# Optimization experiments

Measured on AMD Instinct MI355X. Metric: run time of the kernel, lower is better.

## Reference

```python
import jax, jax.numpy as jnp
import numpy as np

FD, NH, SP, GS = 256, 4, 2, 80.0
E = FD // NH
SP3 = SP ** 3


def _bilinear(plane, uv):
    # plane: [B,C,H,W], uv: [B,N,2] in [0,1] -> [B,C,N] (align_corners=True style)
    B, C, H, W = plane.shape
    x = jnp.clip(uv[..., 0], 0.0, 1.0) * (W - 1)
    y = jnp.clip(uv[..., 1], 0.0, 1.0) * (H - 1)
    x0 = jnp.floor(x); y0 = jnp.floor(y)
    wx = (x - x0)[:, None, :]; wy = (y - y0)[:, None, :]
    x0i = x0.astype(jnp.int32); y0i = y0.astype(jnp.int32)
    x1i = jnp.minimum(x0i + 1, W - 1); y1i = jnp.minimum(y0i + 1, H - 1)
    g = jax.vmap(lambda pl, yy, xx: pl[:, yy, xx])  # per-batch gather -> [C,N]
    f00 = g(plane, y0i, x0i); f01 = g(plane, y0i, x1i)
    f10 = g(plane, y1i, x0i); f11 = g(plane, y1i, x1i)
    return (f00 * (1 - wy) * (1 - wx) + f01 * (1 - wy) * wx
            + f10 * wy * (1 - wx) + f11 * wy * wx)


def _triplane(p, c_xz, c_xy, c_yz):
    # p: [B,N,3] in [0,1] -> [B,N,FD]; sum of three plane samples (ConvONet style)
    px, py, pz = p[..., 0], p[..., 1], p[..., 2]
    f = (_bilinear(c_xz, jnp.stack([px, pz], -1))
         + _bilinear(c_xy, jnp.stack([px, py], -1))
         + _bilinear(c_yz, jnp.stack([py, pz], -1)))
    return jnp.swapaxes(f, 1, 2)


def setup_inputs() -> dict:
    key = jax.random.key(0)
    ks = jax.random.split(key, 10)
    bs, ns, H = 4, 1024, 128
    inp = {}
    inp['query_pos'] = jax.random.uniform(ks[0], (bs, ns, 3), dtype=jnp.float32)
    for i, nm in enumerate(['c_xz', 'c_xy', 'c_yz']):
        inp[nm] = jax.random.normal(ks[1 + i], (bs, FD, H, H), dtype=jnp.float32)

    def lin(k, fi, fo):  # xavier-uniform like torch init
        lim = (6.0 / (fi + fo)) ** 0.5
        return jax.random.uniform(k, (fi, fo), minval=-lim, maxval=lim, dtype=jnp.float32)

    # to_offset: small random weight (torch inits to 0; small noise exercises the path),
    # bias = normalized sp^3 anchor grid / grid_scale, tiled over heads (as in __init__)
    inp['w_off'] = 0.01 * jax.random.normal(ks[4], (FD, SP3 * NH * 3), dtype=jnp.float32)
    g = np.stack(np.meshgrid(np.arange(SP), np.arange(SP), np.arange(SP), indexing='ij'), axis=-1).astype(np.float32)
    gsc = (2.0 * g / max(SP - 1, 1) - 1.0) / GS  # [sp,sp,sp,3]
    inp['b_off'] = jnp.asarray(np.tile(gsc[:, :, :, None, :], (1, 1, 1, NH, 1)).reshape(-1))
    inp['w_q'] = lin(ks[5], FD, E); inp['b_q'] = jnp.zeros((E,), jnp.float32)
    inp['w_k'] = lin(ks[6], FD, E); inp['b_k'] = jnp.zeros((E,), jnp.float32)
    inp['w_v'] = lin(ks[7], FD, E); inp['b_v'] = jnp.zeros((E,), jnp.float32)
    inp['w_out'] = lin(ks[8], FD, FD); inp['b_out'] = jnp.zeros((FD,), jnp.float32)
    return inp


def reference(query_pos, c_xz, c_xy, c_yz, w_off, b_off, w_q, b_q, w_k, b_k, w_v, b_v, w_out, b_out):
    bs, ns, _ = query_pos.shape
    feature = _triplane(query_pos, c_xz, c_xy, c_yz)                 # [bs,ns,FD]
    off = (feature @ w_off + b_off).reshape(bs, ns, SP3, NH, 3)
    aux = off + query_pos[:, :, None, None, :]                        # [bs,ns,SP3,NH,3]
    aux_feat = _triplane(aux.reshape(bs, -1, 3), c_xz, c_xy, c_yz)
    aux_feat = aux_feat.reshape(bs * ns, SP3, NH, FD)
    k = jnp.swapaxes(aux_feat @ w_k + b_k, 1, 2)                      # [bn,NH,SP3,E]
    v = jnp.swapaxes(aux_feat @ w_v + b_v, 1, 2)
    # note: original does q / scale with scale = E**-0.5, i.e. q * sqrt(E)
    q = (feature @ w_q + b_q).reshape(bs * ns, 1, 1, E) * (E ** 0.5)
    q = jnp.broadcast_to(q, (bs * ns, NH, 1, E))
    sim = jnp.einsum('bnid,bnjd->bnij', q, k)                         # [bn,NH,1,SP3]
    attn = jax.nn.softmax(sim, axis=-1)                               # dropout = identity (eval)
    out = jnp.einsum('bnij,bnjd->bnid', attn, v)                      # [bn,NH,1,E]
    out = jnp.swapaxes(out, 1, 2).reshape(bs, ns, NH * E)
    return out @ w_out + b_out + feature
```

## Files before the change

### kernel.cpp

```cpp
#include <hip/hip_runtime.h>
#include <math.h>

#define FD   256
#define NH   4
#define SP3  8
#define NP   32
#define EDIM 64
#define H    128
#define NS   1024
#define BS   4
#define QT   8

#define TEX         (H*H)
#define BATCH_ELEMS (TEX*FD)
#define PAIR_B      2
#define PAIR_Q      (PAIR_B*NS)
#define PPLANE      (PAIR_B*BATCH_ELEMS)

#define WS_PLANES 0
#define WS_FEAT   (3*PPLANE)
#define WS_QK     (WS_FEAT + PAIR_Q*FD)
#define WS_AUX    (WS_QK   + PAIR_Q*FD)
#define WS_WF     (WS_AUX  + PAIR_Q*NP*3)
#define WS_PERM   (WS_WF   + PAIR_Q*NH*FD)

__device__ __forceinline__ unsigned short f2bf(float f) {
  unsigned b = __float_as_uint(f);
  return (unsigned short)((b + 0x7FFFu + ((b >> 16) & 1u)) >> 16);
}
__device__ __forceinline__ float bf2f(unsigned short u) {
  return __uint_as_float(((unsigned)u) << 16);
}

__global__ __launch_bounds__(256) void tpk2(
    const float* __restrict__ xz, const float* __restrict__ xy,
    const float* __restrict__ yz, float* __restrict__ dstAll, int b0)
{
  int bid = blockIdx.x;
  int tT = bid & 511; bid >>= 9;
  int bl = bid & 1;   bid >>= 1;
  int pl = bid;
  const float* src = pl == 0 ? xz : (pl == 1 ? xy : yz);
  float* dst = dstAll + (size_t)pl * PPLANE + (size_t)bl * BATCH_ELEMS;
  int b = b0 + bl;

  __shared__ float T[32 * 260];
  int lane = threadIdx.x & 63, w = threadIdx.x >> 6;
  int tex4 = (lane & 7) * 4;
  int csub = lane >> 3;

  const float* sbase = src + (size_t)b * FD * TEX + tT * 32;
  #pragma unroll
  for (int i = 0; i < 8; i++) {
    int c = i * 32 + w * 8 + csub;
    float4 v = *(const float4*)(sbase + (size_t)c * TEX + tex4);
    T[(tex4 + 0) * 260 + c] = v.x;
    T[(tex4 + 1) * 260 + c] = v.y;
    T[(tex4 + 2) * 260 + c] = v.z;
    T[(tex4 + 3) * 260 + c] = v.w;
  }
  __syncthreads();
  #pragma unroll
  for (int i = 0; i < 8; i++) {
    int t = w * 8 + i;
    float4 v = *(const float4*)(&T[t * 260 + lane * 4]);
    *(float4*)(dst + (size_t)(tT * 32 + t) * FD + lane * 4) = v;
  }
}

__device__ __forceinline__ unsigned mort7(unsigned v) {
  unsigned r = 0;
  #pragma unroll
  for (int i = 0; i < 7; i++) r |= ((v >> i) & 1u) << (3 * i);
  return r;
}

__global__ __launch_bounds__(1024) void sortk(
    const float* __restrict__ qpos, unsigned* __restrict__ perm)
{
  const int pair = blockIdx.x;
  const int b0 = pair * PAIR_B;
  const int t = threadIdx.x;
  __shared__ unsigned cnt[256];
  __shared__ unsigned base[256];
  if (t < 256) cnt[t] = 0;
  __syncthreads();
  unsigned myb[2];
  #pragma unroll
  for (int r = 0; r < 2; r++) {
    int i = t + r * 1024;
    size_t qg = (size_t)b0 * NS + i;
    float x = fminf(fmaxf(qpos[qg * 3 + 0], 0.f), 1.f);
    float y = fminf(fmaxf(qpos[qg * 3 + 1], 0.f), 1.f);
    float z = fminf(fmaxf(qpos[qg * 3 + 2], 0.f), 1.f);
    unsigned m = (mort7((unsigned)(x * 127.f)) << 2)
               | (mort7((unsigned)(y * 127.f)) << 1)
               |  mort7((unsigned)(z * 127.f));
    unsigned bkt = ((unsigned)(i >> 10) << 7) | (m >> 14);
    myb[r] = bkt;
    atomicAdd(&cnt[bkt], 1u);
  }
  __syncthreads();
  if (t == 0) {
    unsigned s = 0;
    for (int k = 0; k < 256; k++) { base[k] = s; s += cnt[k]; }
  }
  __syncthreads();
  #pragma unroll
  for (int r = 0; r < 2; r++) {
    int i = t + r * 1024;
    unsigned pos = atomicAdd(&base[myb[r]], 1u);
    perm[(size_t)pair * PAIR_Q + pos] = (unsigned)i;
  }
}

__device__ __forceinline__ float sample_plane(const float* __restrict__ p,
                                              float u, float v) {
  float x = fminf(fmaxf(u, 0.f), 1.f) * (float)(H - 1);
  float y = fminf(fmaxf(v, 0.f), 1.f) * (float)(H - 1);
  float xf = floorf(x), yf = floorf(y);
  int x0 = (int)xf, y0 = (int)yf;
  float wx = x - xf, wy = y - yf;
  int dx = (x0 < H - 1) ? FD : 0;
  int dy = (y0 < H - 1) ? H * FD : 0;
  int i00 = (y0 * H + x0) * FD;
  float f00 = p[i00], f01 = p[i00 + dx], f10 = p[i00 + dy], f11 = p[i00 + dy + dx];
  float a = f00 + wx * (f01 - f00);
  float b = f10 + wx * (f11 - f10);
  return a + wy * (b - a);
}

__device__ __forceinline__ void setup_samp(int* si, float* sw, float u, float v) {
  float x = fminf(fmaxf(u, 0.f), 1.f) * (float)(H - 1);
  float y = fminf(fmaxf(v, 0.f), 1.f) * (float)(H - 1);
  float xf = floorf(x), yf = floorf(y);
  int x0 = (int)xf, y0 = (int)yf;
  float wx = x - xf, wy = y - yf;
  si[0] = (y0 * H + x0) * FD;
  si[1] = (x0 < H - 1) ? FD : 0;
  si[2] = (y0 < H - 1) ? H * FD : 0;
  sw[0] = (1.f - wy) * (1.f - wx);
  sw[1] = (1.f - wy) * wx;
  sw[2] = wy * (1.f - wx);
  sw[3] = wy * wx;
}

__global__ __launch_bounds__(256) void featk(
    const float* __restrict__ qpos, const float* __restrict__ planesT,
    const float* __restrict__ w_off, const float* __restrict__ b_off,
    const float* __restrict__ w_q, const float* __restrict__ b_q,
    const float* __restrict__ w_k,
    float* __restrict__ feat, float* __restrict__ aux, float* __restrict__ qk,
    int b0)
{
  const int tid = threadIdx.x;
  const int q0l = blockIdx.x * QT;
  const int bl = q0l >> 10;
  __shared__ float s_feat[QT * 260];
  __shared__ float s_q[QT * 68];

  const float* Pxz = planesT + 0 * (size_t)PPLANE + (size_t)bl * BATCH_ELEMS + tid;
  const float* Pxy = planesT + 1 * (size_t)PPLANE + (size_t)bl * BATCH_ELEMS + tid;
  const float* Pyz = planesT + 2 * (size_t)PPLANE + (size_t)bl * BATCH_ELEMS + tid;

  for (int qs = 0; qs < QT; qs++) {
    size_t qg = (size_t)b0 * NS + q0l + qs;
    float px = qpos[qg * 3 + 0], py = qpos[qg * 3 + 1], pz = qpos[qg * 3 + 2];
    float f = sample_plane(Pxz, px, pz) + sample_plane(Pxy, px, py)
            + sample_plane(Pyz, py, pz);
    s_feat[qs * 260 + tid] = f;
    feat[(size_t)(q0l + qs) * FD + tid] = f;
  }
  __syncthreads();

  if (tid < 192) {
    int half = tid / 96, j = tid - half * 96;
    float acc[4];
    float bj = b_off[j];
    #pragma unroll
    for (int k = 0; k < 4; k++) acc[k] = bj;
    for (int c = 0; c < FD; c++) {
      float wv = w_off[c * 96 + j];
      #pragma unroll
      for (int k = 0; k < 4; k++)
        acc[k] = fmaf(s_feat[(half * 4 + k) * 260 + c], wv, acc[k]);
    }
    int d = j % 3;
    #pragma unroll
    for (int k = 0; k < 4; k++) {
      int qs = half * 4 + k;
      size_t qg = (size_t)b0 * NS + q0l + qs;
      aux[(size_t)(q0l + qs) * 96 + j] = acc[k] + qpos[qg * 3 + d];
    }
  }
  {
    int e = tid & 63, g = tid >> 6;
    #pragma unroll
    for (int k = 0; k < 2; k++) {
      int qs = g * 2 + k;
      float a = b_q[e];
      for (int c = 0; c < FD; c++)
        a = fmaf(s_feat[qs * 260 + c], w_q[c * EDIM + e], a);
      s_q[qs * 68 + e] = a * 8.0f;
    }
  }
  __syncthreads();
  {
    float acc[QT];
    #pragma unroll
    for (int qs = 0; qs < QT; qs++) acc[qs] = 0.f;
    const float4* wk4 = reinterpret_cast<const float4*>(w_k + (size_t)tid * EDIM);
    for (int e4 = 0; e4 < EDIM / 4; e4++) {
      float4 wv = wk4[e4];
      int e = e4 * 4;
      #pragma unroll
      for (int qs = 0; qs < QT; qs++) {
        acc[qs] = fmaf(s_q[qs * 68 + e + 0], wv.x, acc[qs]);
        acc[qs] = fmaf(s_q[qs * 68 + e + 1], wv.y, acc[qs]);
        acc[qs] = fmaf(s_q[qs * 68 + e + 2], wv.z, acc[qs]);
        acc[qs] = fmaf(s_q[qs * 68 + e + 3], wv.w, acc[qs]);
      }
    }
    #pragma unroll
    for (int qs = 0; qs < QT; qs++)
      qk[(size_t)(q0l + qs) * FD + tid] = acc[qs];
  }
}

__global__ __launch_bounds__(256) void attnk(
    const float* __restrict__ planesT, const float* __restrict__ aux,
    const float* __restrict__ qk, const unsigned* __restrict__ perm,
    float* __restrict__ wf)
{
  const int tid = threadIdx.x, lane = tid & 63, w = tid >> 6;
  const int bid = blockIdx.x;
  const int j = ((bid & 7) << 7) | (bid >> 3);
  const int c4 = lane * 4;

  __shared__ int     s_si[2][96][3];
  __shared__ float   s_sw[2][96][4];
  __shared__ float   s_sim[2][NP];
  __shared__ float   s_attn[2][NP];
  __shared__ ushort4 s_af[2 * NP * 64];
  __shared__ int     s_q[2];

  if (tid < 2) s_q[tid] = (int)perm[2 * j + tid];
  __syncthreads();
  const int qw = s_q[w >> 1];
  const int blw = qw >> 10;

  if (tid < 192) {
    int qi = tid / 96, r = tid - qi * 96;
    int p = r / 3, pl = r - p * 3;
    int qq = s_q[qi];
    float ax = aux[(size_t)qq * 96 + p * 3 + 0];
    float ay = aux[(size_t)qq * 96 + p * 3 + 1];
    float az = aux[(size_t)qq * 96 + p * 3 + 2];
    float u = (pl == 2) ? ay : ax;
    float v = (pl == 1) ? ay : az;
    setup_samp(s_si[qi][r], s_sw[qi][r], u, v);
  }
  float4 qk4 = *(const float4*)(qk + (size_t)qw * FD + c4);
  const float* P0 = planesT + 0 * (size_t)PPLANE + (size_t)blw * BATCH_ELEMS + c4;
  const float* P1 = planesT + 1 * (size_t)PPLANE + (size_t)blw * BATCH_ELEMS + c4;
  const float* P2 = planesT + 2 * (size_t)PPLANE + (size_t)blw * BATCH_ELEMS + c4;
  __syncthreads();

  const int qi = w >> 1;
  #pragma unroll 2
  for (int k = 0; k < 16; k++) {
    int p = (w & 1) * 16 + k;
    float4 a; a.x = 0.f; a.y = 0.f; a.z = 0.f; a.w = 0.f;
    #pragma unroll
    for (int pl = 0; pl < 3; pl++) {
      const float* P = pl == 0 ? P0 : (pl == 1 ? P1 : P2);
      int i00 = s_si[qi][p * 3 + pl][0];
      int dxo = s_si[qi][p * 3 + pl][1];
      int dyo = s_si[qi][p * 3 + pl][2];
      float w0 = s_sw[qi][p * 3 + pl][0], w1 = s_sw[qi][p * 3 + pl][1];
      float w2 = s_sw[qi][p * 3 + pl][2], w3 = s_sw[qi][p * 3 + pl][3];
      float4 f00 = *(const float4*)(P + i00);
      float4 f01 = *(const float4*)(P + i00 + dxo);
      float4 f10 = *(const float4*)(P + i00 + dyo);
      float4 f11 = *(const float4*)(P + i00 + dyo + dxo);
      a.x = fmaf(w0, f00.x, fmaf(w1, f01.x, fmaf(w2, f10.x, fmaf(w3, f11.x, a.x))));
      a.y = fmaf(w0, f00.y, fmaf(w1, f01.y, fmaf(w2, f10.y, fmaf(w3, f11.y, a.y))));
      a.z = fmaf(w0, f00.z, fmaf(w1, f01.z, fmaf(w2, f10.z, fmaf(w3, f11.z, a.z))));
      a.w = fmaf(w0, f00.w, fmaf(w1, f01.w, fmaf(w2, f10.w, fmaf(w3, f11.w, a.w))));
    }
    ushort4 h;
    h.x = f2bf(a.x); h.y = f2bf(a.y); h.z = f2bf(a.z); h.w = f2bf(a.w);
    s_af[(qi * NP + p) * 64 + lane] = h;
    float t = fmaf(qk4.x, a.x, fmaf(qk4.y, a.y, fmaf(qk4.z, a.z, qk4.w * a.w)));
    #pragma unroll
    for (int o = 32; o >= 1; o >>= 1) t += __shfl_xor(t, o, 64);
    if (lane == 0) s_sim[qi][p] = t;
  }
  __syncthreads();

  if (tid < 2 * NH) {
    int si = tid >> 2, h = tid & 3;
    float sim[SP3], m = -1e30f;
    #pragma unroll
    for (int jj = 0; jj < SP3; jj++) { sim[jj] = s_sim[si][jj * NH + h]; m = fmaxf(m, sim[jj]); }
    float sum = 0.f, e_[SP3];
    #pragma unroll
    for (int jj = 0; jj < SP3; jj++) { e_[jj] = __expf(sim[jj] - m); sum += e_[jj]; }
    float inv = 1.0f / sum;
    #pragma unroll
    for (int jj = 0; jj < SP3; jj++) s_attn[si][jj * NH + h] = e_[jj] * inv;
  }
  __syncthreads();

  {
    #pragma unroll
    for (int hi = 0; hi < 2; hi++) {
      int h = (w & 1) + hi * 2;
      float4 r; r.x = 0.f; r.y = 0.f; r.z = 0.f; r.w = 0.f;
      #pragma unroll
      for (int jj = 0; jj < SP3; jj++) {
        int p = jj * NH + h;
        float a = s_attn[qi][p];
        ushort4 hv = s_af[(qi * NP + p) * 64 + lane];
        r.x = fmaf(a, bf2f(hv.x), r.x);
        r.y = fmaf(a, bf2f(hv.y), r.y);
        r.z = fmaf(a, bf2f(hv.z), r.z);
        r.w = fmaf(a, bf2f(hv.w), r.w);
      }
      *(float4*)(wf + ((size_t)qw * NH + h) * FD + c4) = r;
    }
  }
}

__global__ __launch_bounds__(256) void epik(
    const float* __restrict__ wf, const float* __restrict__ feat,
    const float* __restrict__ w_v, const float* __restrict__ b_v,
    const float* __restrict__ w_out, const float* __restrict__ b_out,
    float* __restrict__ out, int b0)
{
  const int tid = threadIdx.x;
  const int q0l = blockIdx.x * QT;
  __shared__ float s_wv[FD * EDIM];
  __shared__ float s_o[QT * 257];

  {
    const float4* src4 = (const float4*)w_v;
    float4* dst4 = (float4*)s_wv;
    #pragma unroll
    for (int i = 0; i < (FD * EDIM / 4) / 256; i++)
      dst4[tid + 256 * i] = src4[tid + 256 * i];
  }
  __syncthreads();

  {
    int h = tid >> 6, e = tid & 63;
    float acc[QT];
    float bv = b_v[e];
    #pragma unroll
    for (int qs = 0; qs < QT; qs++) acc[qs] = bv;
    const float* wrow = wf + ((size_t)q0l * NH + h) * FD;
    for (int c = 0; c < FD; c++) {
      float wv = s_wv[c * EDIM + e];
      #pragma unroll
      for (int qs = 0; qs < QT; qs++)
        acc[qs] = fmaf(wrow[(size_t)qs * NH * FD + c], wv, acc[qs]);
    }
    #pragma unroll
    for (int qs = 0; qs < QT; qs++) s_o[qs * 257 + h * EDIM + e] = acc[qs];
  }
  __syncthreads();

  {
    float r[QT];
    float bo = b_out[tid];
    #pragma unroll
    for (int qs = 0; qs < QT; qs++) r[qs] = bo;
    for (int c = 0; c < FD; c++) {
      float wv = w_out[(size_t)c * FD + tid];
      #pragma unroll
      for (int qs = 0; qs < QT; qs++)
        r[qs] = fmaf(s_o[qs * 257 + c], wv, r[qs]);
    }
    #pragma unroll
    for (int qs = 0; qs < QT; qs++)
      out[((size_t)b0 * NS + q0l + qs) * FD + tid]
          = r[qs] + feat[(size_t)(q0l + qs) * FD + tid];
  }
}

extern "C" void kernel_launch(void* const* d_in, const int* in_sizes, int n_in,
                              void* d_out, int out_size, void* d_ws, size_t ws_size,
                              hipStream_t stream) {
  const float* qp    = (const float*)d_in[0];
  const float* cxz   = (const float*)d_in[1];
  const float* cxy   = (const float*)d_in[2];
  const float* cyz   = (const float*)d_in[3];
  const float* w_off = (const float*)d_in[4];
  const float* b_off = (const float*)d_in[5];
  const float* w_q   = (const float*)d_in[6];
  const float* b_q   = (const float*)d_in[7];
  const float* w_k   = (const float*)d_in[8];
  const float* b_k   = (const float*)d_in[9];   (void)b_k;
  const float* w_v   = (const float*)d_in[10];
  const float* b_v   = (const float*)d_in[11];
  const float* w_out = (const float*)d_in[12];
  const float* b_out = (const float*)d_in[13];
  float* out = (float*)d_out;
  (void)in_sizes; (void)n_in; (void)out_size; (void)ws_size;

  float* ws      = (float*)d_ws;
  float* planesT = ws + WS_PLANES;
  float* feat    = ws + WS_FEAT;
  float* qk      = ws + WS_QK;
  float* aux     = ws + WS_AUX;
  float* wf      = ws + WS_WF;
  unsigned* perm = (unsigned*)(ws + WS_PERM);

  hipLaunchKernelGGL(sortk, dim3(BS / PAIR_B), dim3(1024), 0, stream, qp, perm);

  for (int pair = 0; pair < BS / PAIR_B; ++pair) {
    int b0 = pair * PAIR_B;
    hipLaunchKernelGGL(tpk2, dim3(3 * PAIR_B * 512), dim3(256), 0, stream,
                       cxz, cxy, cyz, planesT, b0);
    hipLaunchKernelGGL(featk, dim3(PAIR_Q / QT), dim3(256), 0, stream,
                       qp, planesT, w_off, b_off, w_q, b_q, w_k,
                       feat, aux, qk, b0);
    hipLaunchKernelGGL(attnk, dim3(PAIR_Q / 2), dim3(256), 0, stream,
                       planesT, aux, qk, perm + (size_t)pair * PAIR_Q, wf);
    hipLaunchKernelGGL(epik, dim3(PAIR_Q / QT), dim3(256), 0, stream,
                       wf, feat, w_v, b_v, w_out, b_out, out, b0);
  }
}
```

Baseline: 538.9 us.

## Restructure attention kernel to per-wave softmax in registers, shrink query tiles

The attention kernel now has each wave handle one query's head pair end to end. It keeps the bf16 samples and similarity scores in registers and computes the softmax locally, which removes the shared-memory staging buffers and two block-wide barriers. It also adds a min-blocks-per-CU launch bound to raise occupancy. The feature and epilogue kernels halve their per-block query tile from 8 to 4, doubling the grid size at the cost of less weight reuse per block. The register-resident arrays could raise register pressure or cause spills under the occupancy bound.

```diff
diff --git a/kernel.cpp b/kernel.cpp
--- a/kernel.cpp
+++ b/kernel.cpp
@@ -9,7 +9,8 @@
 #define H    128
 #define NS   1024
 #define BS   4
-#define QT   8
+#define QTF  4
+#define QTE  4
 
 #define TEX         (H*H)
 #define BATCH_ELEMS (TEX*FD)
@@ -154,16 +155,16 @@
     int b0)
 {
   const int tid = threadIdx.x;
-  const int q0l = blockIdx.x * QT;
+  const int q0l = blockIdx.x * QTF;
   const int bl = q0l >> 10;
-  __shared__ float s_feat[QT * 260];
-  __shared__ float s_q[QT * 68];
+  __shared__ float s_feat[QTF * 260];
+  __shared__ float s_q[QTF * 68];
 
   const float* Pxz = planesT + 0 * (size_t)PPLANE + (size_t)bl * BATCH_ELEMS + tid;
   const float* Pxy = planesT + 1 * (size_t)PPLANE + (size_t)bl * BATCH_ELEMS + tid;
   const float* Pyz = planesT + 2 * (size_t)PPLANE + (size_t)bl * BATCH_ELEMS + tid;
 
-  for (int qs = 0; qs < QT; qs++) {
+  for (int qs = 0; qs < QTF; qs++) {
     size_t qg = (size_t)b0 * NS + q0l + qs;
     float px = qpos[qg * 3 + 0], py = qpos[qg * 3 + 1], pz = qpos[qg * 3 + 2];
     float f = sample_plane(Pxz, px, pz) + sample_plane(Pxy, px, py)
@@ -175,46 +176,41 @@
 
   if (tid < 192) {
     int half = tid / 96, j = tid - half * 96;
-    float acc[4];
+    float acc[2];
     float bj = b_off[j];
-    #pragma unroll
-    for (int k = 0; k < 4; k++) acc[k] = bj;
+    acc[0] = bj; acc[1] = bj;
     for (int c = 0; c < FD; c++) {
       float wv = w_off[c * 96 + j];
       #pragma unroll
-      for (int k = 0; k < 4; k++)
-        acc[k] = fmaf(s_feat[(half * 4 + k) * 260 + c], wv, acc[k]);
+      for (int k = 0; k < 2; k++)
+        acc[k] = fmaf(s_feat[(half * 2 + k) * 260 + c], wv, acc[k]);
     }
     int d = j % 3;
     #pragma unroll
-    for (int k = 0; k < 4; k++) {
-      int qs = half * 4 + k;
+    for (int k = 0; k < 2; k++) {
+      int qs = half * 2 + k;
       size_t qg = (size_t)b0 * NS + q0l + qs;
       aux[(size_t)(q0l + qs) * 96 + j] = acc[k] + qpos[qg * 3 + d];
     }
   }
   {
     int e = tid & 63, g = tid >> 6;
-    #pragma unroll
-    for (int k = 0; k < 2; k++) {
-      int qs = g * 2 + k;
-      float a = b_q[e];
-      for (int c = 0; c < FD; c++)
-        a = fmaf(s_feat[qs * 260 + c], w_q[c * EDIM + e], a);
-      s_q[qs * 68 + e] = a * 8.0f;
-    }
+    float a = b_q[e];
+    for (int c = 0; c < FD; c++)
+      a = fmaf(s_feat[g * 260 + c], w_q[c * EDIM + e], a);
+    s_q[g * 68 + e] = a * 8.0f;
   }
   __syncthreads();
   {
-    float acc[QT];
-    #pragma unroll
-    for (int qs = 0; qs < QT; qs++) acc[qs] = 0.f;
+    float acc[QTF];
+    #pragma unroll
+    for (int qs = 0; qs < QTF; qs++) acc[qs] = 0.f;
     const float4* wk4 = reinterpret_cast<const float4*>(w_k + (size_t)tid * EDIM);
     for (int e4 = 0; e4 < EDIM / 4; e4++) {
       float4 wv = wk4[e4];
       int e = e4 * 4;
       #pragma unroll
-      for (int qs = 0; qs < QT; qs++) {
+      for (int qs = 0; qs < QTF; qs++) {
         acc[qs] = fmaf(s_q[qs * 68 + e + 0], wv.x, acc[qs]);
         acc[qs] = fmaf(s_q[qs * 68 + e + 1], wv.y, acc[qs]);
         acc[qs] = fmaf(s_q[qs * 68 + e + 2], wv.z, acc[qs]);
@@ -222,12 +218,12 @@
       }
     }
     #pragma unroll
-    for (int qs = 0; qs < QT; qs++)
+    for (int qs = 0; qs < QTF; qs++)
       qk[(size_t)(q0l + qs) * FD + tid] = acc[qs];
   }
 }
 
-__global__ __launch_bounds__(256) void attnk(
+__global__ __launch_bounds__(256, 6) void attnk(
     const float* __restrict__ planesT, const float* __restrict__ aux,
     const float* __restrict__ qk, const unsigned* __restrict__ perm,
     float* __restrict__ wf)
@@ -237,98 +233,83 @@
   const int j = ((bid & 7) << 7) | (bid >> 3);
   const int c4 = lane * 4;
 
-  __shared__ int     s_si[2][96][3];
-  __shared__ float   s_sw[2][96][4];
-  __shared__ float   s_sim[2][NP];
-  __shared__ float   s_attn[2][NP];
-  __shared__ ushort4 s_af[2 * NP * 64];
-  __shared__ int     s_q[2];
-
-  if (tid < 2) s_q[tid] = (int)perm[2 * j + tid];
-  __syncthreads();
-  const int qw = s_q[w >> 1];
-  const int blw = qw >> 10;
+  __shared__ int   s_si[2][96][3];
+  __shared__ float s_sw[2][96][4];
 
   if (tid < 192) {
-    int qi = tid / 96, r = tid - qi * 96;
+    int qi_s = tid / 96, r = tid - qi_s * 96;
     int p = r / 3, pl = r - p * 3;
-    int qq = s_q[qi];
+    int qq = (int)perm[2 * j + qi_s];
     float ax = aux[(size_t)qq * 96 + p * 3 + 0];
     float ay = aux[(size_t)qq * 96 + p * 3 + 1];
     float az = aux[(size_t)qq * 96 + p * 3 + 2];
     float u = (pl == 2) ? ay : ax;
     float v = (pl == 1) ? ay : az;
-    setup_samp(s_si[qi][r], s_sw[qi][r], u, v);
-  }
+    setup_samp(s_si[qi_s][r], s_sw[qi_s][r], u, v);
+  }
+
+  const int qi = w >> 1;
+  const int h0 = w & 1;
+  const int qw = (int)perm[2 * j + qi];
+  const int blw = qw >> 10;
   float4 qk4 = *(const float4*)(qk + (size_t)qw * FD + c4);
   const float* P0 = planesT + 0 * (size_t)PPLANE + (size_t)blw * BATCH_ELEMS + c4;
   const float* P1 = planesT + 1 * (size_t)PPLANE + (size_t)blw * BATCH_ELEMS + c4;
   const float* P2 = planesT + 2 * (size_t)PPLANE + (size_t)blw * BATCH_ELEMS + c4;
   __syncthreads();
 
-  const int qi = w >> 1;
-  #pragma unroll 2
-  for (int k = 0; k < 16; k++) {
-    int p = (w & 1) * 16 + k;
-    float4 a; a.x = 0.f; a.y = 0.f; a.z = 0.f; a.w = 0.f;
-    #pragma unroll
-    for (int pl = 0; pl < 3; pl++) {
-      const float* P = pl == 0 ? P0 : (pl == 1 ? P1 : P2);
-      int i00 = s_si[qi][p * 3 + pl][0];
-      int dxo = s_si[qi][p * 3 + pl][1];
-      int dyo = s_si[qi][p * 3 + pl][2];
-      float w0 = s_sw[qi][p * 3 + pl][0], w1 = s_sw[qi][p * 3 + pl][1];
-      float w2 = s_sw[qi][p * 3 + pl][2], w3 = s_sw[qi][p * 3 + pl][3];
-      float4 f00 = *(const float4*)(P + i00);
-      float4 f01 = *(const float4*)(P + i00 + dxo);
-      float4 f10 = *(const float4*)(P + i00 + dyo);
-      float4 f11 = *(const float4*)(P + i00 + dyo + dxo);
-      a.x = fmaf(w0, f00.x, fmaf(w1, f01.x, fmaf(w2, f10.x, fmaf(w3, f11.x, a.x))));
-      a.y = fmaf(w0, f00.y, fmaf(w1, f01.y, fmaf(w2, f10.y, fmaf(w3, f11.y, a.y))));
-      a.z = fmaf(w0, f00.z, fmaf(w1, f01.z, fmaf(w2, f10.z, fmaf(w3, f11.z, a.z))));
-      a.w = fmaf(w0, f00.w, fmaf(w1, f01.w, fmaf(w2, f10.w, fmaf(w3, f11.w, a.w))));
-    }
-    ushort4 h;
-    h.x = f2bf(a.x); h.y = f2bf(a.y); h.z = f2bf(a.z); h.w = f2bf(a.w);
-    s_af[(qi * NP + p) * 64 + lane] = h;
-    float t = fmaf(qk4.x, a.x, fmaf(qk4.y, a.y, fmaf(qk4.z, a.z, qk4.w * a.w)));
-    #pragma unroll
-    for (int o = 32; o >= 1; o >>= 1) t += __shfl_xor(t, o, 64);
-    if (lane == 0) s_sim[qi][p] = t;
-  }
-  __syncthreads();
-
-  if (tid < 2 * NH) {
-    int si = tid >> 2, h = tid & 3;
-    float sim[SP3], m = -1e30f;
-    #pragma unroll
-    for (int jj = 0; jj < SP3; jj++) { sim[jj] = s_sim[si][jj * NH + h]; m = fmaxf(m, sim[jj]); }
-    float sum = 0.f, e_[SP3];
-    #pragma unroll
-    for (int jj = 0; jj < SP3; jj++) { e_[jj] = __expf(sim[jj] - m); sum += e_[jj]; }
+  #pragma unroll
+  for (int hi = 0; hi < 2; hi++) {
+    const int h = h0 + 2 * hi;
+    ushort4 af16[SP3];
+    float sim[SP3];
+    #pragma unroll 2
+    for (int jj = 0; jj < SP3; jj++) {
+      const int p = jj * NH + h;
+      float4 a; a.x = 0.f; a.y = 0.f; a.z = 0.f; a.w = 0.f;
+      #pragma unroll
+      for (int pl = 0; pl < 3; pl++) {
+        const float* P = pl == 0 ? P0 : (pl == 1 ? P1 : P2);
+        int i00 = s_si[qi][p * 3 + pl][0];
+        int dxo = s_si[qi][p * 3 + pl][1];
+        int dyo = s_si[qi][p * 3 + pl][2];
+        float w0 = s_sw[qi][p * 3 + pl][0], w1 = s_sw[qi][p * 3 + pl][1];
+        float w2 = s_sw[qi][p * 3 + pl][2], w3 = s_sw[qi][p * 3 + pl][3];
+        float4 f00 = *(const float4*)(P + i00);
+        float4 f01 = *(const float4*)(P + i00 + dxo);
+        float4 f10 = *(const float4*)(P + i00 + dyo);
+        float4 f11 = *(const float4*)(P + i00 + dyo + dxo);
+        a.x = fmaf(w0, f00.x, fmaf(w1, f01.x, fmaf(w2, f10.x, fmaf(w3, f11.x, a.x))));
+        a.y = fmaf(w0, f00.y, fmaf(w1, f01.y, fmaf(w2, f10.y, fmaf(w3, f11.y, a.y))));
+        a.z = fmaf(w0, f00.z, fmaf(w1, f01.z, fmaf(w2, f10.z, fmaf(w3, f11.z, a.z))));
+        a.w = fmaf(w0, f00.w, fmaf(w1, f01.w, fmaf(w2, f10.w, fmaf(w3, f11.w, a.w))));
+      }
+      ushort4 hh;
+      hh.x = f2bf(a.x); hh.y = f2bf(a.y); hh.z = f2bf(a.z); hh.w = f2bf(a.w);
+      af16[jj] = hh;
+      float t = fmaf(qk4.x, a.x, fmaf(qk4.y, a.y, fmaf(qk4.z, a.z, qk4.w * a.w)));
+      #pragma unroll
+      for (int o = 32; o >= 1; o >>= 1) t += __shfl_xor(t, o, 64);
+      sim[jj] = t;
+    }
+    float m = -1e30f;
+    #pragma unroll
+    for (int jj = 0; jj < SP3; jj++) m = fmaxf(m, sim[jj]);
+    float sum = 0.f;
+    #pragma unroll
+    for (int jj = 0; jj < SP3; jj++) { sim[jj] = __expf(sim[jj] - m); sum += sim[jj]; }
     float inv = 1.0f / sum;
-    #pragma unroll
-    for (int jj = 0; jj < SP3; jj++) s_attn[si][jj * NH + h] = e_[jj] * inv;
-  }
-  __syncthreads();
-
-  {
-    #pragma unroll
-    for (int hi = 0; hi < 2; hi++) {
-      int h = (w & 1) + hi * 2;
-      float4 r; r.x = 0.f; r.y = 0.f; r.z = 0.f; r.w = 0.f;
-      #pragma unroll
-      for (int jj = 0; jj < SP3; jj++) {
-        int p = jj * NH + h;
-        float a = s_attn[qi][p];
-        ushort4 hv = s_af[(qi * NP + p) * 64 + lane];
-        r.x = fmaf(a, bf2f(hv.x), r.x);
-        r.y = fmaf(a, bf2f(hv.y), r.y);
-        r.z = fmaf(a, bf2f(hv.z), r.z);
-        r.w = fmaf(a, bf2f(hv.w), r.w);
-      }
-      *(float4*)(wf + ((size_t)qw * NH + h) * FD + c4) = r;
-    }
+    float4 r; r.x = 0.f; r.y = 0.f; r.z = 0.f; r.w = 0.f;
+    #pragma unroll
+    for (int jj = 0; jj < SP3; jj++) {
+      float av = sim[jj] * inv;
+      ushort4 hv = af16[jj];
+      r.x = fmaf(av, bf2f(hv.x), r.x);
+      r.y = fmaf(av, bf2f(hv.y), r.y);
+      r.z = fmaf(av, bf2f(hv.z), r.z);
+      r.w = fmaf(av, bf2f(hv.w), r.w);
+    }
+    *(float4*)(wf + ((size_t)qw * NH + h) * FD + c4) = r;
   }
 }
 
@@ -339,9 +320,9 @@
     float* __restrict__ out, int b0)
 {
   const int tid = threadIdx.x;
-  const int q0l = blockIdx.x * QT;
+  const int q0l = blockIdx.x * QTE;
   __shared__ float s_wv[FD * EDIM];
-  __shared__ float s_o[QT * 257];
+  __shared__ float s_o[QTE * 257];
 
   {
     const float4* src4 = (const float4*)w_v;
@@ -354,35 +335,35 @@
 
   {
     int h = tid >> 6, e = tid & 63;
-    float acc[QT];
+    float acc[QTE];
     float bv = b_v[e];
     #pragma unroll
-    for (int qs = 0; qs < QT; qs++) acc[qs] = bv;
+    for (int qs = 0; qs < QTE; qs++) acc[qs] = bv;
     const float* wrow = wf + ((size_t)q0l * NH + h) * FD;
     for (int c = 0; c < FD; c++) {
       float wv = s_wv[c * EDIM + e];
       #pragma unroll
-      for (int qs = 0; qs < QT; qs++)
+      for (int qs = 0; qs < QTE; qs++)
         acc[qs] = fmaf(wrow[(size_t)qs * NH * FD + c], wv, acc[qs]);
     }
     #pragma unroll
-    for (int qs = 0; qs < QT; qs++) s_o[qs * 257 + h * EDIM + e] = acc[qs];
+    for (int qs = 0; qs < QTE; qs++) s_o[qs * 257 + h * EDIM + e] = acc[qs];
   }
   __syncthreads();
 
   {
-    float r[QT];
+    float r[QTE];
     float bo = b_out[tid];
     #pragma unroll
-    for (int qs = 0; qs < QT; qs++) r[qs] = bo;
+    for (int qs = 0; qs < QTE; qs++) r[qs] = bo;
     for (int c = 0; c < FD; c++) {
       float wv = w_out[(size_t)c * FD + tid];
       #pragma unroll
-      for (int qs = 0; qs < QT; qs++)
+      for (int qs = 0; qs < QTE; qs++)
         r[qs] = fmaf(s_o[qs * 257 + c], wv, r[qs]);
     }
     #pragma unroll
-    for (int qs = 0; qs < QT; qs++)
+    for (int qs = 0; qs < QTE; qs++)
       out[((size_t)b0 * NS + q0l + qs) * FD + tid]
           = r[qs] + feat[(size_t)(q0l + qs) * FD + tid];
   }
@@ -422,12 +403,12 @@
     int b0 = pair * PAIR_B;
     hipLaunchKernelGGL(tpk2, dim3(3 * PAIR_B * 512), dim3(256), 0, stream,
                        cxz, cxy, cyz, planesT, b0);
-    hipLaunchKernelGGL(featk, dim3(PAIR_Q / QT), dim3(256), 0, stream,
+    hipLaunchKernelGGL(featk, dim3(PAIR_Q / QTF), dim3(256), 0, stream,
                        qp, planesT, w_off, b_off, w_q, b_q, w_k,
                        feat, aux, qk, b0);
     hipLaunchKernelGGL(attnk, dim3(PAIR_Q / 2), dim3(256), 0, stream,
                        planesT, aux, qk, perm + (size_t)pair * PAIR_Q, wf);
-    hipLaunchKernelGGL(epik, dim3(PAIR_Q / QT), dim3(256), 0, stream,
+    hipLaunchKernelGGL(epik, dim3(PAIR_Q / QTE), dim3(256), 0, stream,
                        wf, feat, w_v, b_v, w_out, b_out, out, b0);
   }
 }
```

Result: no change. 531.7 us (-1.3%).
